# Kernel tuning notes

Measured on AMD Instinct MI355X. Metric: run time of the kernel, lower is better.

The kernel has to match this reference:

```python
import jax, jax.numpy as jnp
import numpy as np
import math

D_MODEL = 1024
N_HEADS = 16
D_HEAD = D_MODEL // N_HEADS
B, S = 4, 2048


def setup_inputs() -> dict:
    key = jax.random.key(0)
    ks = jax.random.split(key, 9)
    std = 1.0 / math.sqrt(D_MODEL)
    x = jax.random.normal(ks[0], (B, S, D_MODEL), dtype=jnp.float32)
    # causal mask: True = masked out
    mask = jnp.triu(jnp.ones((S, S), dtype=bool), k=1)
    Wq = jax.random.normal(ks[1], (D_MODEL, D_MODEL), jnp.float32) * std
    bq = jnp.zeros((D_MODEL,), jnp.float32)
    Wk = jax.random.normal(ks[2], (D_MODEL, D_MODEL), jnp.float32) * std
    bk = jnp.zeros((D_MODEL,), jnp.float32)
    Wv = jax.random.normal(ks[3], (D_MODEL, D_MODEL), jnp.float32) * std
    bv = jnp.zeros((D_MODEL,), jnp.float32)
    Wo = jax.random.normal(ks[4], (D_MODEL, D_MODEL), jnp.float32) * std
    bo = jnp.zeros((D_MODEL,), jnp.float32)
    return {"x": x, "mask": mask, "Wq": Wq, "bq": bq, "Wk": Wk, "bk": bk,
            "Wv": Wv, "bv": bv, "Wo": Wo, "bo": bo}


def reference(x, mask, Wq, bq, Wk, bk, Wv, bv, Wo, bo):
    b, s, _ = x.shape
    scale = math.sqrt(D_HEAD)
    # projections (Linear: x @ W.T + b), reshape to [b, h, s, d]
    def proj(W, bias):
        y = jnp.einsum('bsd,ed->bse', x, W) + bias
        return y.reshape(b, s, N_HEADS, D_HEAD).transpose(0, 2, 1, 3)
    q = proj(Wq, bq)
    k = proj(Wk, bk)
    v = proj(Wv, bv)
    scores = jnp.einsum('bhqd,bhkd->bhqk', q, k) / scale  # [b,h,s,s]
    scores = jnp.where(mask[None, None, :, :], -jnp.inf, scores)
    attn = jax.nn.softmax(scores, axis=-1)
    # dropout is identity in eval mode
    out = jnp.einsum('bhqk,bhkd->bhqd', attn, v)
    out = out.transpose(0, 2, 1, 3).reshape(b, s, D_MODEL)
    return jnp.einsum('bsd,ed->bse', out, Wo) + bo
```

## Files before the change

### kernel.cpp

```cpp
#include <hip/hip_runtime.h>
#include <stdint.h>

#define NH 16
#define DH 64
#define DM 1024
#define Bz 4
#define Sz 2048

typedef __bf16 bf16x8 __attribute__((ext_vector_type(8)));
typedef float f32x4 __attribute__((ext_vector_type(4)));

#define GLD_LDS16(gsrc, ldst)                                             \
    __builtin_amdgcn_global_load_lds(                                     \
        (const __attribute__((address_space(1))) void*)(gsrc),            \
        (__attribute__((address_space(3))) void*)(ldst), 16, 0, 0)

__device__ __forceinline__ unsigned short f2bf(float f) {
    unsigned u = __float_as_uint(f);
    u += 0x7FFFu + ((u >> 16) & 1u);
    return (unsigned short)(u >> 16);
}
__device__ __forceinline__ float bf2f(unsigned short h) {
    return __uint_as_float(((unsigned)h) << 16);
}

__global__ void detect_dtype(const unsigned short* __restrict__ xs,
                             int* __restrict__ flagp)
{
    const int t = threadIdx.x;
    int cnt = 0;
    for (int i = 0; i < 64; i++) {
        const unsigned short h = xs[(t * 64 + i) * 2];
        const int e = (h >> 7) & 0xFF;
        if (h != 0 && e >= 100 && e <= 130) cnt++;
    }
#pragma unroll
    for (int off = 32; off >= 1; off >>= 1)
        cnt += __shfl_xor(cnt, off);
    if (t == 0) *flagp = (cnt < 2048) ? 1 : 0;
}

__global__ __launch_bounds__(256) void convert_inputs(
    const void* s0, const void* s1, const void* s2, const void* s3,
    const void* s4, const void* s5, const void* s6, const void* s7,
    const void* s8,
    unsigned short* d0, unsigned short* d1, unsigned short* d2,
    unsigned short* d3, unsigned short* d4, unsigned short* d5,
    unsigned short* d6, unsigned short* d7, unsigned short* d8,
    const int* __restrict__ flagp)
{
    const void* s; unsigned short* d; int n;
    switch (blockIdx.y) {
        case 0: s = s0; d = d0; n = Bz * Sz * DM; break;
        case 1: s = s1; d = d1; n = DM * DM; break;
        case 2: s = s2; d = d2; n = DM * DM; break;
        case 3: s = s3; d = d3; n = DM * DM; break;
        case 4: s = s4; d = d4; n = DM * DM; break;
        case 5: s = s5; d = d5; n = DM; break;
        case 6: s = s6; d = d6; n = DM; break;
        case 7: s = s7; d = d7; n = DM; break;
        default: s = s8; d = d8; n = DM; break;
    }
    const int flag   = *flagp;
    const int stride = gridDim.x * blockDim.x * 4;
    const int base   = (blockIdx.x * blockDim.x + threadIdx.x) * 4;
    if (flag) {
        const float* sf = (const float*)s;
        for (int i = base; i < n; i += stride) {
            const float4 v = *reinterpret_cast<const float4*>(&sf[i]);
            ushort2 a, b;
            a.x = f2bf(v.x); a.y = f2bf(v.y);
            b.x = f2bf(v.z); b.y = f2bf(v.w);
            *reinterpret_cast<ushort2*>(&d[i])     = a;
            *reinterpret_cast<ushort2*>(&d[i + 2]) = b;
        }
    } else {
        const unsigned short* sh = (const unsigned short*)s;
        for (int i = base; i < n; i += stride)
            *reinterpret_cast<uint2*>(&d[i]) = *reinterpret_cast<const uint2*>(&sh[i]);
    }
}

__global__ __launch_bounds__(256) void gemm_qkv(
    const unsigned short* __restrict__ X,
    const unsigned short* __restrict__ Wq,
    const unsigned short* __restrict__ Wk,
    const unsigned short* __restrict__ Wv,
    const unsigned short* __restrict__ bq,
    const unsigned short* __restrict__ bk,
    const unsigned short* __restrict__ bv,
    unsigned short* __restrict__ Qb,
    unsigned short* __restrict__ Kb,
    unsigned short* __restrict__ Vtb)
{
    __shared__ __align__(16) unsigned short As[2][128 * 32];
    __shared__ __align__(16) unsigned short Bs[2][128 * 32];
    const int tid  = threadIdx.x;
    const int w    = tid >> 6, lane = tid & 63;
    const int quad = lane >> 4, l15 = lane & 15;
    const int wm   = (w & 1) * 64, wn = (w >> 1) * 64;
    const int bm   = blockIdx.y * 128;
    const int proj = blockIdx.x >> 3;
    const int bn   = (blockIdx.x & 7) * 128;

    const unsigned short* W      = proj == 0 ? Wq : (proj == 1 ? Wk : Wv);
    const unsigned short* bias_p = proj == 0 ? bq : (proj == 1 ? bk : bv);

    const int lrow = lane >> 2;
    const int lcol = (lane & 3) * 8;

    f32x4 acc[4][4];
    for (int i = 0; i < 4; i++)
        for (int j = 0; j < 4; j++)
            acc[i][j] = f32x4{0.f, 0.f, 0.f, 0.f};

    for (int kk = 0; kk < DM; kk += 64) {
        __syncthreads();
#pragma unroll
        for (int s2 = 0; s2 < 2; s2++) {
#pragma unroll
            for (int t = 0; t < 2; t++) {
                const int r = w * 32 + t * 16;
                GLD_LDS16(&X[(size_t)(bm + r + lrow) * DM + kk + s2 * 32 + lcol], &As[s2][r * 32]);
                GLD_LDS16(&W[(size_t)(bn + r + lrow) * DM + kk + s2 * 32 + lcol], &Bs[s2][r * 32]);
            }
        }
        asm volatile("s_waitcnt vmcnt(0)" ::: "memory");
        __syncthreads();

#pragma unroll
        for (int s2 = 0; s2 < 2; s2++) {
            bf16x8 af[4], bfr[4];
#pragma unroll
            for (int i = 0; i < 4; i++)
                af[i] = *reinterpret_cast<const bf16x8*>(&As[s2][(wm + i * 16 + l15) * 32 + quad * 8]);
#pragma unroll
            for (int j = 0; j < 4; j++)
                bfr[j] = *reinterpret_cast<const bf16x8*>(&Bs[s2][(wn + j * 16 + l15) * 32 + quad * 8]);
#pragma unroll
            for (int i = 0; i < 4; i++)
#pragma unroll
                for (int j = 0; j < 4; j++)
                    acc[i][j] = __builtin_amdgcn_mfma_f32_16x16x32_bf16(af[i], bfr[j], acc[i][j], 0, 0, 0);
        }
    }

    if (proj < 2) {
        unsigned short* dst = (proj == 0) ? Qb : Kb;
#pragma unroll
        for (int j = 0; j < 4; j++) {
            const int   e    = bn + wn + j * 16 + l15;
            const int   h    = e >> 6, dd = e & 63;
            const float bias = bf2f(bias_p[e]);
#pragma unroll
            for (int i = 0; i < 4; i++) {
#pragma unroll
                for (int r = 0; r < 4; r++) {
                    const int m = bm + wm + i * 16 + quad * 4 + r;
                    const int b = m >> 11, s = m & 2047;
                    dst[((size_t)(b * NH + h) * Sz + s) * DH + dd] = f2bf(acc[i][j][r] + bias);
                }
            }
        }
    } else {
#pragma unroll
        for (int j = 0; j < 4; j++) {
            const int   e    = bn + wn + j * 16 + l15;
            const int   h    = e >> 6, dd = e & 63;
            const float bias = bf2f(bias_p[e]);
#pragma unroll
            for (int i = 0; i < 4; i++) {
                const int m0 = bm + wm + i * 16 + quad * 4;
                const int b  = m0 >> 11, s0 = m0 & 2047;
                const unsigned u0 = __float_as_uint(acc[i][j][0] + bias) + 0x8000u;
                const unsigned u1 = __float_as_uint(acc[i][j][1] + bias) + 0x8000u;
                const unsigned u2 = __float_as_uint(acc[i][j][2] + bias) + 0x8000u;
                const unsigned u3 = __float_as_uint(acc[i][j][3] + bias) + 0x8000u;
                uint2 pk;
                pk.x = __builtin_amdgcn_perm(u1, u0, 0x07060302u);
                pk.y = __builtin_amdgcn_perm(u3, u2, 0x07060302u);
                *reinterpret_cast<uint2*>(
                    &Vtb[((size_t)(b * NH + h) * DH + dd) * Sz + s0]) = pk;
            }
        }
    }
}

__global__ __launch_bounds__(512) void flash_attn(
    const unsigned short* __restrict__ Qb,
    const unsigned short* __restrict__ Kb,
    const unsigned short* __restrict__ Vtb,
    unsigned short* __restrict__ AOb)
{
    __shared__ __align__(16) unsigned short Ks[64 * 72];
    __shared__ __align__(16) unsigned short Vs[64 * 72];
    __shared__ __align__(16) unsigned short Ps[128 * 72];

    const int tid  = threadIdx.x;
    const int w    = tid >> 6, lane = tid & 63;
    const int quad = lane >> 4, l15 = lane & 15;
    const int bh   = blockIdx.y;
    const int cA   = (int)(blockIdx.x & 7);

    const int srow = tid >> 3;
    const int scc  = (tid & 7) * 8;
    const int hh = bh & 15, bb = bh >> 4;

    for (int pass = 0; pass < 2; pass++) {
        const int chunk = pass ? (15 - cA) : cA;
        const int qb = chunk * 128;
        const int qw = qb + w * 16;

        const size_t qbase = ((size_t)bh * Sz + qw + l15) * DH;
        const bf16x8 qf0 = *reinterpret_cast<const bf16x8*>(&Qb[qbase + quad * 8]);
        const bf16x8 qf1 = *reinterpret_cast<const bf16x8*>(&Qb[qbase + 32 + quad * 8]);

        f32x4 o[4];
#pragma unroll
        for (int jd = 0; jd < 4; jd++) o[jd] = f32x4{0.f, 0.f, 0.f, 0.f};
        float lsum = 0.f;

        const int n_kv = qb + 128;

        for (int kb = 0; kb < n_kv; kb += 64) {
            __syncthreads();
            *reinterpret_cast<uint4*>(&Ks[srow * 72 + scc]) =
                *reinterpret_cast<const uint4*>(&Kb[((size_t)bh * Sz + kb + srow) * DH + scc]);
            *reinterpret_cast<uint4*>(&Vs[srow * 72 + scc]) =
                *reinterpret_cast<const uint4*>(&Vtb[((size_t)bh * DH + srow) * Sz + kb + scc]);
            __syncthreads();

            if (kb > qw + 15) continue;
            const bool need_mask = (kb + 64 > qw);

#pragma unroll
            for (int j = 0; j < 4; j++) {
                const bf16x8 kf0 = *reinterpret_cast<const bf16x8*>(&Ks[(j * 16 + l15) * 72 + quad * 8]);
                const bf16x8 kf1 = *reinterpret_cast<const bf16x8*>(&Ks[(j * 16 + l15) * 72 + 32 + quad * 8]);
                f32x4 st = f32x4{0.f, 0.f, 0.f, 0.f};
                st = __builtin_amdgcn_mfma_f32_16x16x32_bf16(kf0, qf0, st, 0, 0, 0);
                st = __builtin_amdgcn_mfma_f32_16x16x32_bf16(kf1, qf1, st, 0, 0, 0);
                const int qa = qw + l15;
                float p[4];
#pragma unroll
                for (int r = 0; r < 4; r++) {
                    float e = __builtin_amdgcn_exp2f(st[r] * 0.18033688011f);
                    if (need_mask) {
                        const int kv = kb + j * 16 + quad * 4 + r;
                        e = (kv <= qa) ? e : 0.f;
                    }
                    p[r] = e;
                }
                lsum += (p[0] + p[1]) + (p[2] + p[3]);
                const unsigned u0 = __float_as_uint(p[0]) + 0x8000u;
                const unsigned u1 = __float_as_uint(p[1]) + 0x8000u;
                const unsigned u2 = __float_as_uint(p[2]) + 0x8000u;
                const unsigned u3 = __float_as_uint(p[3]) + 0x8000u;
                const unsigned pk0 = __builtin_amdgcn_perm(u1, u0, 0x07060302u);
                const unsigned pk1 = __builtin_amdgcn_perm(u3, u2, 0x07060302u);
                const int prow = (w * 16 + l15) * 72 + j * 16 + quad * 4;
                *reinterpret_cast<unsigned*>(&Ps[prow])     = pk0;
                *reinterpret_cast<unsigned*>(&Ps[prow + 2]) = pk1;
            }

            asm volatile("s_waitcnt lgkmcnt(0)" ::: "memory");

            const bf16x8 pf0 = *reinterpret_cast<const bf16x8*>(&Ps[(w * 16 + l15) * 72 + quad * 8]);
            const bf16x8 pf1 = *reinterpret_cast<const bf16x8*>(&Ps[(w * 16 + l15) * 72 + 32 + quad * 8]);
#pragma unroll
            for (int jd = 0; jd < 4; jd++) {
                const bf16x8 vf0 = *reinterpret_cast<const bf16x8*>(&Vs[(jd * 16 + l15) * 72 + quad * 8]);
                const bf16x8 vf1 = *reinterpret_cast<const bf16x8*>(&Vs[(jd * 16 + l15) * 72 + 32 + quad * 8]);
                o[jd] = __builtin_amdgcn_mfma_f32_16x16x32_bf16(pf0, vf0, o[jd], 0, 0, 0);
                o[jd] = __builtin_amdgcn_mfma_f32_16x16x32_bf16(pf1, vf1, o[jd], 0, 0, 0);
            }
        }

        lsum += __shfl_xor(lsum, 16);
        lsum += __shfl_xor(lsum, 32);

        float linv[4];
#pragma unroll
        for (int r = 0; r < 4; r++)
            linv[r] = 1.0f / __shfl(lsum, quad * 4 + r);
#pragma unroll
        for (int jd = 0; jd < 4; jd++) {
#pragma unroll
            for (int r = 0; r < 4; r++) {
                const int s = qw + quad * 4 + r;
                AOb[((size_t)(bb * Sz + s)) * DM + hh * DH + jd * 16 + l15] =
                    f2bf(o[jd][r] * linv[r]);
            }
        }
    }
}

__global__ __launch_bounds__(256) void gemm_out(
    const unsigned short* __restrict__ A,
    const unsigned short* __restrict__ W,
    const unsigned short* __restrict__ bo,
    void* __restrict__ outv,
    const int* __restrict__ flagp)
{
    __shared__ __align__(16) unsigned short As[2][128 * 32];
    __shared__ __align__(16) unsigned short Bs[2][128 * 32];
    const int tid  = threadIdx.x;
    const int w    = tid >> 6, lane = tid & 63;
    const int quad = lane >> 4, l15 = lane & 15;
    const int wm   = (w & 1) * 64, wn = (w >> 1) * 64;
    const int bm   = blockIdx.y * 128;
    const int bn   = blockIdx.x * 128;

    const int lrow = lane >> 2;
    const int lcol = (lane & 3) * 8;

    f32x4 acc[4][4];
    for (int i = 0; i < 4; i++)
        for (int j = 0; j < 4; j++)
            acc[i][j] = f32x4{0.f, 0.f, 0.f, 0.f};

    for (int kk = 0; kk < DM; kk += 64) {
        __syncthreads();
#pragma unroll
        for (int s2 = 0; s2 < 2; s2++) {
#pragma unroll
            for (int t = 0; t < 2; t++) {
                const int r = w * 32 + t * 16;
                GLD_LDS16(&A[(size_t)(bm + r + lrow) * DM + kk + s2 * 32 + lcol], &As[s2][r * 32]);
                GLD_LDS16(&W[(size_t)(bn + r + lrow) * DM + kk + s2 * 32 + lcol], &Bs[s2][r * 32]);
            }
        }
        asm volatile("s_waitcnt vmcnt(0)" ::: "memory");
        __syncthreads();

#pragma unroll
        for (int s2 = 0; s2 < 2; s2++) {
            bf16x8 af[4], bfr[4];
#pragma unroll
            for (int i = 0; i < 4; i++)
                af[i] = *reinterpret_cast<const bf16x8*>(&As[s2][(wm + i * 16 + l15) * 32 + quad * 8]);
#pragma unroll
            for (int j = 0; j < 4; j++)
                bfr[j] = *reinterpret_cast<const bf16x8*>(&Bs[s2][(wn + j * 16 + l15) * 32 + quad * 8]);
#pragma unroll
            for (int i = 0; i < 4; i++)
#pragma unroll
                for (int j = 0; j < 4; j++)
                    acc[i][j] = __builtin_amdgcn_mfma_f32_16x16x32_bf16(af[i], bfr[j], acc[i][j], 0, 0, 0);
        }
    }

    const int flag = *flagp;
    float*          outf = (float*)outv;
    unsigned short* outh = (unsigned short*)outv;
#pragma unroll
    for (int j = 0; j < 4; j++) {
        const int   e    = bn + wn + j * 16 + l15;
        const float bias = bf2f(bo[e]);
#pragma unroll
        for (int i = 0; i < 4; i++) {
#pragma unroll
            for (int r = 0; r < 4; r++) {
                const int   m = bm + wm + i * 16 + quad * 4 + r;
                const float v = acc[i][j][r] + bias;
                if (flag) outf[(size_t)m * DM + e] = v;
                else      outh[(size_t)m * DM + e] = f2bf(v);
            }
        }
    }
}

extern "C" void kernel_launch(void* const* d_in, const int* in_sizes, int n_in,
                              void* d_out, int out_size, void* d_ws, size_t ws_size,
                              hipStream_t stream) {
    const void* x = nullptr;
    const void* Wsrc[4] = {nullptr, nullptr, nullptr, nullptr};
    const void* bsrc[4] = {nullptr, nullptr, nullptr, nullptr};
    int nw = 0, nb = 0;
    for (int i = 0; i < n_in; i++) {
        const int sz = in_sizes[i];
        if (sz == Bz * Sz * DM)            { if (!x) x = d_in[i]; }
        else if (sz == DM * DM)            { if (nw < 4) Wsrc[nw++] = d_in[i]; }
        else if (sz == DM)                 { if (nb < 4) bsrc[nb++] = d_in[i]; }
    }

    char* wsb = (char*)d_ws;
    int*  flagp = (int*)wsb;
    unsigned short* Xc  = (unsigned short*)(wsb + 16);
    const size_t NX = (size_t)Bz * Sz * DM;
    const size_t NW = (size_t)DM * DM;
    unsigned short* Wc0 = Xc  + NX;
    unsigned short* Wc1 = Wc0 + NW;
    unsigned short* Wc2 = Wc1 + NW;
    unsigned short* Wc3 = Wc2 + NW;
    unsigned short* bc0 = Wc3 + NW;
    unsigned short* bc1 = bc0 + DM;
    unsigned short* bc2 = bc1 + DM;
    unsigned short* bc3 = bc2 + DM;
    unsigned short* Qb  = bc3 + DM;
    const size_t SZ = (size_t)Bz * NH * Sz * DH;
    unsigned short* Kb  = Qb  + SZ;
    unsigned short* Vtb = Kb  + SZ;
    unsigned short* AOb = Vtb + SZ;

    detect_dtype<<<1, 64, 0, stream>>>((const unsigned short*)x, flagp);
    convert_inputs<<<dim3(512, 9), 256, 0, stream>>>(
        x, Wsrc[0], Wsrc[1], Wsrc[2], Wsrc[3],
        bsrc[0], bsrc[1], bsrc[2], bsrc[3],
        Xc, Wc0, Wc1, Wc2, Wc3, bc0, bc1, bc2, bc3, flagp);

    gemm_qkv <<<dim3(24, 64), 256, 0, stream>>>(Xc, Wc0, Wc1, Wc2, bc0, bc1, bc2, Qb, Kb, Vtb);
    flash_attn<<<dim3(8, 64), 512, 0, stream>>>(Qb, Kb, Vtb, AOb);
    gemm_out <<<dim3(8, 64), 256, 0, stream>>>(AOb, Wc3, bc3, d_out, flagp);
}
```

Before: 323.5 us.

## Double-buffer GEMM K-tiles and register-prefetch K/V in attention loop

The QKV projection and output GEMMs now stage 32-wide K slices into two LDS buffers, issuing the next slice's global-to-LDS loads before computing on the current one. Previously each 64-wide step loaded synchronously and then computed. The attention kernel prefetches the next 64-row K/V tile into registers while the current tile is computed from LDS, unrolled by two. This hides global memory latency behind MFMA work, at the cost of twice as many barriers per K step in the GEMMs and extra registers for the prefetched tiles.

```diff
diff --git a/kernel.cpp b/kernel.cpp
--- a/kernel.cpp
+++ b/kernel.cpp
@@ -114,36 +114,41 @@
         for (int j = 0; j < 4; j++)
             acc[i][j] = f32x4{0.f, 0.f, 0.f, 0.f};
 
-    for (int kk = 0; kk < DM; kk += 64) {
-        __syncthreads();
-#pragma unroll
-        for (int s2 = 0; s2 < 2; s2++) {
-#pragma unroll
-            for (int t = 0; t < 2; t++) {
-                const int r = w * 32 + t * 16;
-                GLD_LDS16(&X[(size_t)(bm + r + lrow) * DM + kk + s2 * 32 + lcol], &As[s2][r * 32]);
-                GLD_LDS16(&W[(size_t)(bn + r + lrow) * DM + kk + s2 * 32 + lcol], &Bs[s2][r * 32]);
-            }
-        }
+    auto stage = [&](int buf, int ks) {
+        const int k0 = ks << 5;
+#pragma unroll
+        for (int t = 0; t < 2; t++) {
+            const int r = w * 32 + t * 16;
+            GLD_LDS16(&X[(size_t)(bm + r + lrow) * DM + k0 + lcol], &As[buf][r * 32]);
+            GLD_LDS16(&W[(size_t)(bn + r + lrow) * DM + k0 + lcol], &Bs[buf][r * 32]);
+        }
+    };
+
+    auto compute32 = [&](int cur) {
+        bf16x8 af[4], bfr[4];
+#pragma unroll
+        for (int i = 0; i < 4; i++)
+            af[i] = *reinterpret_cast<const bf16x8*>(&As[cur][(wm + i * 16 + l15) * 32 + quad * 8]);
+#pragma unroll
+        for (int j = 0; j < 4; j++)
+            bfr[j] = *reinterpret_cast<const bf16x8*>(&Bs[cur][(wn + j * 16 + l15) * 32 + quad * 8]);
+#pragma unroll
+        for (int i = 0; i < 4; i++)
+#pragma unroll
+            for (int j = 0; j < 4; j++)
+                acc[i][j] = __builtin_amdgcn_mfma_f32_16x16x32_bf16(af[i], bfr[j], acc[i][j], 0, 0, 0);
+    };
+
+    stage(0, 0);
+    asm volatile("s_waitcnt vmcnt(0)" ::: "memory");
+    __syncthreads();
+    for (int t = 0; t < 31; ++t) {
+        stage((t + 1) & 1, t + 1);
+        compute32(t & 1);
         asm volatile("s_waitcnt vmcnt(0)" ::: "memory");
         __syncthreads();
-
-#pragma unroll
-        for (int s2 = 0; s2 < 2; s2++) {
-            bf16x8 af[4], bfr[4];
-#pragma unroll
-            for (int i = 0; i < 4; i++)
-                af[i] = *reinterpret_cast<const bf16x8*>(&As[s2][(wm + i * 16 + l15) * 32 + quad * 8]);
-#pragma unroll
-            for (int j = 0; j < 4; j++)
-                bfr[j] = *reinterpret_cast<const bf16x8*>(&Bs[s2][(wn + j * 16 + l15) * 32 + quad * 8]);
-#pragma unroll
-            for (int i = 0; i < 4; i++)
-#pragma unroll
-                for (int j = 0; j < 4; j++)
-                    acc[i][j] = __builtin_amdgcn_mfma_f32_16x16x32_bf16(af[i], bfr[j], acc[i][j], 0, 0, 0);
-        }
-    }
+    }
+    compute32(1);
 
     if (proj < 2) {
         unsigned short* dst = (proj == 0) ? Qb : Kb;
@@ -222,17 +227,8 @@
 
         const int n_kv = qb + 128;
 
-        for (int kb = 0; kb < n_kv; kb += 64) {
-            __syncthreads();
-            *reinterpret_cast<uint4*>(&Ks[srow * 72 + scc]) =
-                *reinterpret_cast<const uint4*>(&Kb[((size_t)bh * Sz + kb + srow) * DH + scc]);
-            *reinterpret_cast<uint4*>(&Vs[srow * 72 + scc]) =
-                *reinterpret_cast<const uint4*>(&Vtb[((size_t)bh * DH + srow) * Sz + kb + scc]);
-            __syncthreads();
-
-            if (kb > qw + 15) continue;
+        auto compute = [&](int kb) {
             const bool need_mask = (kb + 64 > qw);
-
 #pragma unroll
             for (int j = 0; j < 4; j++) {
                 const bf16x8 kf0 = *reinterpret_cast<const bf16x8*>(&Ks[(j * 16 + l15) * 72 + quad * 8]);
@@ -274,6 +270,34 @@
                 o[jd] = __builtin_amdgcn_mfma_f32_16x16x32_bf16(pf0, vf0, o[jd], 0, 0, 0);
                 o[jd] = __builtin_amdgcn_mfma_f32_16x16x32_bf16(pf1, vf1, o[jd], 0, 0, 0);
             }
+        };
+
+        uint4 kr0 = *reinterpret_cast<const uint4*>(&Kb[((size_t)bh * Sz + srow) * DH + scc]);
+        uint4 vr0 = *reinterpret_cast<const uint4*>(&Vtb[((size_t)bh * DH + srow) * Sz + scc]);
+        uint4 kr1, vr1;
+
+        for (int kb = 0; kb < n_kv; kb += 128) {
+            __syncthreads();
+            *reinterpret_cast<uint4*>(&Ks[srow * 72 + scc]) = kr0;
+            *reinterpret_cast<uint4*>(&Vs[srow * 72 + scc]) = vr0;
+            kr1 = *reinterpret_cast<const uint4*>(&Kb[((size_t)bh * Sz + kb + 64 + srow) * DH + scc]);
+            vr1 = *reinterpret_cast<const uint4*>(&Vtb[((size_t)bh * DH + srow) * Sz + kb + 64 + scc]);
+            asm volatile("s_waitcnt lgkmcnt(0)" ::: "memory");
+            __builtin_amdgcn_s_barrier();
+            asm volatile("" ::: "memory");
+            if (kb <= qw + 15) compute(kb);
+
+            __syncthreads();
+            *reinterpret_cast<uint4*>(&Ks[srow * 72 + scc]) = kr1;
+            *reinterpret_cast<uint4*>(&Vs[srow * 72 + scc]) = vr1;
+            if (kb + 128 < n_kv) {
+                kr0 = *reinterpret_cast<const uint4*>(&Kb[((size_t)bh * Sz + kb + 128 + srow) * DH + scc]);
+                vr0 = *reinterpret_cast<const uint4*>(&Vtb[((size_t)bh * DH + srow) * Sz + kb + 128 + scc]);
+            }
+            asm volatile("s_waitcnt lgkmcnt(0)" ::: "memory");
+            __builtin_amdgcn_s_barrier();
+            asm volatile("" ::: "memory");
+            if (kb + 64 <= qw + 15) compute(kb + 64);
         }
 
         lsum += __shfl_xor(lsum, 16);
@@ -319,36 +343,41 @@
         for (int j = 0; j < 4; j++)
             acc[i][j] = f32x4{0.f, 0.f, 0.f, 0.f};
 
-    for (int kk = 0; kk < DM; kk += 64) {
-        __syncthreads();
-#pragma unroll
-        for (int s2 = 0; s2 < 2; s2++) {
-#pragma unroll
-            for (int t = 0; t < 2; t++) {
-                const int r = w * 32 + t * 16;
-                GLD_LDS16(&A[(size_t)(bm + r + lrow) * DM + kk + s2 * 32 + lcol], &As[s2][r * 32]);
-                GLD_LDS16(&W[(size_t)(bn + r + lrow) * DM + kk + s2 * 32 + lcol], &Bs[s2][r * 32]);
-            }
-        }
+    auto stage = [&](int buf, int ks) {
+        const int k0 = ks << 5;
+#pragma unroll
+        for (int t = 0; t < 2; t++) {
+            const int r = w * 32 + t * 16;
+            GLD_LDS16(&A[(size_t)(bm + r + lrow) * DM + k0 + lcol], &As[buf][r * 32]);
+            GLD_LDS16(&W[(size_t)(bn + r + lrow) * DM + k0 + lcol], &Bs[buf][r * 32]);
+        }
+    };
+
+    auto compute32 = [&](int cur) {
+        bf16x8 af[4], bfr[4];
+#pragma unroll
+        for (int i = 0; i < 4; i++)
+            af[i] = *reinterpret_cast<const bf16x8*>(&As[cur][(wm + i * 16 + l15) * 32 + quad * 8]);
+#pragma unroll
+        for (int j = 0; j < 4; j++)
+            bfr[j] = *reinterpret_cast<const bf16x8*>(&Bs[cur][(wn + j * 16 + l15) * 32 + quad * 8]);
+#pragma unroll
+        for (int i = 0; i < 4; i++)
+#pragma unroll
+            for (int j = 0; j < 4; j++)
+                acc[i][j] = __builtin_amdgcn_mfma_f32_16x16x32_bf16(af[i], bfr[j], acc[i][j], 0, 0, 0);
+    };
+
+    stage(0, 0);
+    asm volatile("s_waitcnt vmcnt(0)" ::: "memory");
+    __syncthreads();
+    for (int t = 0; t < 31; ++t) {
+        stage((t + 1) & 1, t + 1);
+        compute32(t & 1);
         asm volatile("s_waitcnt vmcnt(0)" ::: "memory");
         __syncthreads();
-
-#pragma unroll
-        for (int s2 = 0; s2 < 2; s2++) {
-            bf16x8 af[4], bfr[4];
-#pragma unroll
-            for (int i = 0; i < 4; i++)
-                af[i] = *reinterpret_cast<const bf16x8*>(&As[s2][(wm + i * 16 + l15) * 32 + quad * 8]);
-#pragma unroll
-            for (int j = 0; j < 4; j++)
-                bfr[j] = *reinterpret_cast<const bf16x8*>(&Bs[s2][(wn + j * 16 + l15) * 32 + quad * 8]);
-#pragma unroll
-            for (int i = 0; i < 4; i++)
-#pragma unroll
-                for (int j = 0; j < 4; j++)
-                    acc[i][j] = __builtin_amdgcn_mfma_f32_16x16x32_bf16(af[i], bfr[j], acc[i][j], 0, 0, 0);
-        }
-    }
+    }
+    compute32(1);
 
     const int flag = *flagp;
     float*          outf = (float*)outv;
```

Result: slower. 332.4 us (+2.8%).
